# Kernel tuning notes

Measured on AMD Instinct MI355X. Metric: run time of the kernel, lower is better.

## Reference

```python
import jax, jax.numpy as jnp
import numpy as np

N = 8192      # tokens
DIM = 1024    # model dim
E = 8         # num_experts
TOPK = 2      # min(2, num_experts)


def setup_inputs() -> dict:
    key = jax.random.key(0)
    ks = jax.random.split(key, 6)
    def w(k, shape, fan_in):
        return jax.random.normal(k, shape, jnp.float32) / np.float32(np.sqrt(fan_in))
    return {
        "x":   jax.random.normal(ks[0], (N, DIM), jnp.float32),
        # gate MLP: Linear(dim, 2*dim) -> SiLU -> Linear(2*dim, E)
        "Wg1": w(ks[1], (DIM, 2 * DIM), DIM),
        "bg1": jnp.zeros((2 * DIM,), jnp.float32),
        "Wg2": w(ks[2], (2 * DIM, E), 2 * DIM),
        "bg2": jnp.zeros((E,), jnp.float32),
        # experts: SHARED ff1 Linear(dim, 4*dim), per-expert ff2 Linear(4*dim, dim)
        "W1":  w(ks[3], (DIM, 4 * DIM), DIM),
        "b1":  jnp.zeros((4 * DIM,), jnp.float32),
        "W2":  w(ks[4], (E, 4 * DIM, DIM), 4 * DIM),
        "b2":  jnp.zeros((E, DIM), jnp.float32),
    }


def reference(x, Wg1, bg1, Wg2, bg2, W1, b1, W2, b2):
    # gate runs on detached input (x.detach())
    xg = jax.lax.stop_gradient(x)
    gates = jax.nn.silu(xg @ Wg1 + bg1) @ Wg2 + bg2          # [N, E]
    w, idx = jax.lax.top_k(gates, TOPK)                       # [N, K]
    w = jax.nn.softmax(w, axis=-1)                            # softmax over top-k weights
    # shared ff1 hidden, computed once for all experts
    h = jax.nn.silu(x @ W1 + b1)                              # [N, 4*DIM]
    # dense per-expert ff2 over the whole batch (matches original's full-batch expert compute)
    eo = jnp.einsum('nh,ehd->ned', h, W2) + b2                # [N, E, DIM]
    # dispatch/combine: gather selected experts per token, weight and sum
    sel = jnp.take_along_axis(eo, idx[:, :, None], axis=1)    # [N, K, DIM]
    return jnp.sum(w[:, :, None] * sel, axis=1)               # [N, DIM]
```

## Files before the change

### kernel.cpp

```cpp
#include <hip/hip_runtime.h>
#include <hip/hip_bf16.h>
#include <cstddef>

#define N_TOK 8192
#define DIM   1024
#define HG    2048
#define NE    8
#define HEXP  4096

#define BM 128
#define BN 128
#define BK 16
#define THETA 0.05f

typedef __attribute__((ext_vector_type(8))) short bf16x8;
typedef __attribute__((ext_vector_type(4))) float f32x4;

__device__ __forceinline__ float silu_f(float z) {
    return z / (1.0f + expf(-z));
}

__device__ __forceinline__ unsigned short f2bf(float v) {
    unsigned u = __float_as_uint(v);
    unsigned r = (u + 0x7FFFu + ((u >> 16) & 1u)) >> 16;
    return (unsigned short)r;
}

__device__ __forceinline__ float bf2f(unsigned short v) {
    return __uint_as_float((unsigned)v << 16);
}

__device__ __forceinline__ void gl16(const unsigned short* g, unsigned short* l) {
    __builtin_amdgcn_global_load_lds(
        (const __attribute__((address_space(1))) unsigned int*)(const void*)g,
        (__attribute__((address_space(3))) unsigned int*)(void*)l, 16, 0, 0);
}


__global__ __launch_bounds__(256) void conv_x(const float* __restrict__ src,
                                              unsigned short* __restrict__ dst)
{
    const size_t total = (size_t)N_TOK * DIM;
    size_t i = ((size_t)blockIdx.x * 256 + threadIdx.x) * 4;
    const size_t step = (size_t)gridDim.x * 256 * 4;
    for (; i + 3 < total; i += step) {
        float4 v = *(const float4*)(src + i);
        ushort4 o;
        o.x = f2bf(v.x); o.y = f2bf(v.y); o.z = f2bf(v.z); o.w = f2bf(v.w);
        *(ushort4*)(dst + i) = o;
    }
}

__global__ __launch_bounds__(256) void transpose_conv(const float* __restrict__ src,
                                                      unsigned short* __restrict__ dst,
                                                      int R, int C)
{
    __shared__ float tile[64][65];
    const size_t bofs = (size_t)blockIdx.z * R * C;
    const float* s = src + bofs;
    unsigned short* d = dst + bofs;
    const int r0 = blockIdx.y * 64, c0 = blockIdx.x * 64;
    const int t = threadIdx.x;
    #pragma unroll
    for (int i = 0; i < 16; i++) {
        int id = t + i * 256;
        int r = id >> 6, c = id & 63;
        tile[r][c] = s[(size_t)(r0 + r) * C + c0 + c];
    }
    __syncthreads();
    #pragma unroll
    for (int i = 0; i < 16; i++) {
        int id = t + i * 256;
        int c = id >> 6, r = id & 63;
        d[(size_t)(c0 + c) * R + r0 + r] = f2bf(tile[r][c]);
    }
}


#define TBK 64

__global__ __launch_bounds__(256) void gemm_bf16_silu(
    const unsigned short* __restrict__ A,
    const unsigned short* __restrict__ Bt,
    const float* __restrict__ bias,
    unsigned short* __restrict__ C,
    int Nc)
{
    __shared__ __align__(16) unsigned short As[128][TBK];
    __shared__ __align__(16) unsigned short Bs[128][TBK];

    const int tid  = threadIdx.x;
    const int wave = tid >> 6;
    const int lane = tid & 63;
    const int wm = wave >> 1, wn = wave & 1;
    const int l15 = lane & 15;
    const int lk  = lane >> 4;
    const int row0 = blockIdx.y * 128;
    const int col0 = blockIdx.x * 128;

    const int l8  = lane >> 3;
    const int cbs = (lane & 7) ^ l8;
    const unsigned short* pA[4];
    const unsigned short* pB[4];
    #pragma unroll
    for (int i = 0; i < 4; i++) {
        const int r = wave * 32 + i * 8 + l8;
        pA[i] = A  + (size_t)(row0 + r) * DIM + cbs * 8;
        pB[i] = Bt + (size_t)(col0 + r) * DIM + cbs * 8;
    }

    f32x4 acc[4][4] = {};

    for (int k0 = 0; k0 < DIM; k0 += TBK) {
        __syncthreads();
        #pragma unroll
        for (int i = 0; i < 4; i++) {
            gl16(pA[i] + k0, &As[wave * 32 + i * 8][0]);
            gl16(pB[i] + k0, &Bs[wave * 32 + i * 8][0]);
        }
        __syncthreads();

        #pragma unroll
        for (int ks = 0; ks < 2; ks++) {
            bf16x8 af[4], bfr[4];
            const int kb = (ks * 32 + lk * 8) * 2;
            #pragma unroll
            for (int mi = 0; mi < 4; mi++) {
                const int r = wm * 64 + mi * 16 + l15;
                af[mi] = *(const bf16x8*)((const char*)&As[r][0] + (kb ^ ((r & 7) << 4)));
            }
            #pragma unroll
            for (int ni = 0; ni < 4; ni++) {
                const int r = wn * 64 + ni * 16 + l15;
                bfr[ni] = *(const bf16x8*)((const char*)&Bs[r][0] + (kb ^ ((r & 7) << 4)));
            }
            #pragma unroll
            for (int mi = 0; mi < 4; mi++)
                #pragma unroll
                for (int ni = 0; ni < 4; ni++)
                    acc[mi][ni] = __builtin_amdgcn_mfma_f32_16x16x32_bf16(
                        af[mi], bfr[ni], acc[mi][ni], 0, 0, 0);
        }
    }

    #pragma unroll
    for (int ni = 0; ni < 4; ni++) {
        const int gc = col0 + wn * 64 + ni * 16 + l15;
        const float bv = bias[gc];
        #pragma unroll
        for (int mi = 0; mi < 4; mi++) {
            #pragma unroll
            for (int r = 0; r < 4; r++) {
                const int gr = row0 + wm * 64 + mi * 16 + lk * 4 + r;
                C[(size_t)gr * Nc + gc] = f2bf(silu_f(acc[mi][ni][r] + bv));
            }
        }
    }
}


__global__ __launch_bounds__(256) void gate2_topk_flag(
    const unsigned short* __restrict__ g1b, const float* __restrict__ Wg2,
    const float* __restrict__ bg2,
    unsigned* __restrict__ tok_list, float* __restrict__ w_list,
    unsigned* __restrict__ meta, unsigned* __restrict__ flaglist)
{
    const int wid  = threadIdx.x >> 6;
    const int lane = threadIdx.x & 63;
    const int t = blockIdx.x * 4 + wid;
    if (t >= N_TOK) return;

    float acc[NE];
    #pragma unroll
    for (int e = 0; e < NE; e++) acc[e] = 0.0f;

    const unsigned short* g = g1b + (size_t)t * HG;
    for (int kb = lane * 8; kb < HG; kb += 512) {
        ushort4 ga = *(const ushort4*)(g + kb);
        ushort4 gb = *(const ushort4*)(g + kb + 4);
        float gv[8];
        gv[0] = bf2f(ga.x); gv[1] = bf2f(ga.y); gv[2] = bf2f(ga.z); gv[3] = bf2f(ga.w);
        gv[4] = bf2f(gb.x); gv[5] = bf2f(gb.y); gv[6] = bf2f(gb.z); gv[7] = bf2f(gb.w);
        #pragma unroll
        for (int j = 0; j < 8; j++) {
            const float4 wa = *(const float4*)(Wg2 + (size_t)(kb + j) * NE);
            const float4 wb = *(const float4*)(Wg2 + (size_t)(kb + j) * NE + 4);
            acc[0] = fmaf(gv[j], wa.x, acc[0]);
            acc[1] = fmaf(gv[j], wa.y, acc[1]);
            acc[2] = fmaf(gv[j], wa.z, acc[2]);
            acc[3] = fmaf(gv[j], wa.w, acc[3]);
            acc[4] = fmaf(gv[j], wb.x, acc[4]);
            acc[5] = fmaf(gv[j], wb.y, acc[5]);
            acc[6] = fmaf(gv[j], wb.z, acc[6]);
            acc[7] = fmaf(gv[j], wb.w, acc[7]);
        }
    }
    #pragma unroll
    for (int off = 32; off > 0; off >>= 1) {
        #pragma unroll
        for (int e = 0; e < NE; e++)
            acc[e] += __shfl_down(acc[e], off);
    }
    if (lane == 0) {
        float v0 = -3.4e38f, v1 = -3.4e38f, v2 = -3.4e38f;
        int i0 = 0, i1 = 0;
        #pragma unroll
        for (int e = 0; e < NE; e++) {
            const float v = acc[e] + bg2[e];
            if (v > v0)      { v2 = v1; v1 = v0; i1 = i0; v0 = v; i0 = e; }
            else if (v > v1) { v2 = v1; v1 = v; i1 = e; }
            else if (v > v2) { v2 = v; }
        }
        if (v1 - v2 < THETA) {
            const unsigned p = atomicAdd(&meta[17], 1u);
            flaglist[p] = (unsigned)t;
        } else {
            const float e1 = expf(v1 - v0);
            const float inv = 1.0f / (1.0f + e1);
            const unsigned p0 = atomicAdd(&meta[i0], 1u);
            tok_list[i0 * N_TOK + p0] = (unsigned)t;
            w_list [i0 * N_TOK + p0] = inv;
            const unsigned p1 = atomicAdd(&meta[i1], 1u);
            tok_list[i1 * N_TOK + p1] = (unsigned)t;
            w_list [i1 * N_TOK + p1] = e1 * inv;
        }
    }
}

__global__ __launch_bounds__(256) void regate_gemm(
    const float* __restrict__ x, const float* __restrict__ Wg1,
    const float* __restrict__ bg1,
    const unsigned* __restrict__ flaglist, const unsigned* __restrict__ meta,
    float* __restrict__ g1f)
{
    const int nflag = (int)meta[17];
    const int rs = blockIdx.y * BM;
    if (rs >= nflag) return;
    const int re = (rs + BM < nflag) ? rs + BM : nflag;
    const int col0 = blockIdx.x * BN;

    __shared__ float As[BK][BM];
    __shared__ float Bs[BK][BN];

    const int tid = threadIdx.x;
    const int tx = tid & 15;
    const int ty = tid >> 4;
    const int ar = tid >> 2;
    const int ac = (tid & 3) << 2;
    const int br = tid >> 5;
    const int bc = (tid & 31) << 2;

    const int r0 = rs + ar;
    const int r1 = rs + ar + 64;
    const unsigned t0 = flaglist[(r0 < re) ? r0 : rs];
    const unsigned t1 = flaglist[(r1 < re) ? r1 : rs];
    const float* A0 = x + (size_t)t0 * DIM + ac;
    const float* A1 = x + (size_t)t1 * DIM + ac;
    const float* Bp = Wg1 + (size_t)br * HG + col0 + bc;

    float acc[8][8];
    #pragma unroll
    for (int i = 0; i < 8; i++)
        #pragma unroll
        for (int j = 0; j < 8; j++) acc[i][j] = 0.0f;

    for (int k0 = 0; k0 < DIM; k0 += BK) {
        const float4 a0 = *(const float4*)(A0 + k0);
        const float4 a1 = *(const float4*)(A1 + k0);
        const float4 b0 = *(const float4*)(Bp + (size_t)k0 * HG);
        const float4 b1 = *(const float4*)(Bp + (size_t)(k0 + 8) * HG);

        __syncthreads();
        As[ac + 0][ar] = a0.x; As[ac + 1][ar] = a0.y;
        As[ac + 2][ar] = a0.z; As[ac + 3][ar] = a0.w;
        As[ac + 0][ar + 64] = a1.x; As[ac + 1][ar + 64] = a1.y;
        As[ac + 2][ar + 64] = a1.z; As[ac + 3][ar + 64] = a1.w;
        *(float4*)&Bs[br][bc]     = b0;
        *(float4*)&Bs[br + 8][bc] = b1;
        __syncthreads();

        #pragma unroll
        for (int k = 0; k < BK; k++) {
            float a[8], b[8];
            *(float4*)&a[0] = *(const float4*)&As[k][ty * 8];
            *(float4*)&a[4] = *(const float4*)&As[k][ty * 8 + 4];
            *(float4*)&b[0] = *(const float4*)&Bs[k][tx * 8];
            *(float4*)&b[4] = *(const float4*)&Bs[k][tx * 8 + 4];
            #pragma unroll
            for (int i = 0; i < 8; i++)
                #pragma unroll
                for (int j = 0; j < 8; j++)
                    acc[i][j] = fmaf(a[i], b[j], acc[i][j]);
        }
    }

    #pragma unroll
    for (int i = 0; i < 8; i++) {
        const int row = rs + ty * 8 + i;
        if (row < re) {
            const int col = col0 + tx * 8;
            #pragma unroll
            for (int j = 0; j < 8; j++)
                g1f[(size_t)row * HG + col + j] = silu_f(acc[i][j] + bg1[col + j]);
        }
    }
}

__global__ __launch_bounds__(256) void regate_top2(
    const float* __restrict__ g1f, const float* __restrict__ Wg2,
    const float* __restrict__ bg2,
    const unsigned* __restrict__ flaglist,
    unsigned* __restrict__ tok_list, float* __restrict__ w_list,
    unsigned* __restrict__ meta)
{
    const int wid  = threadIdx.x >> 6;
    const int lane = threadIdx.x & 63;
    const int f = blockIdx.x * 4 + wid;
    const int nflag = (int)meta[17];
    if (f >= nflag) return;
    const unsigned t = flaglist[f];

    float acc[NE];
    #pragma unroll
    for (int e = 0; e < NE; e++) acc[e] = 0.0f;

    const float* g = g1f + (size_t)f * HG;
    for (int k = lane; k < HG; k += 64) {
        const float gv = g[k];
        const float4 wa = *(const float4*)(Wg2 + (size_t)k * NE);
        const float4 wb = *(const float4*)(Wg2 + (size_t)k * NE + 4);
        acc[0] = fmaf(gv, wa.x, acc[0]);
        acc[1] = fmaf(gv, wa.y, acc[1]);
        acc[2] = fmaf(gv, wa.z, acc[2]);
        acc[3] = fmaf(gv, wa.w, acc[3]);
        acc[4] = fmaf(gv, wb.x, acc[4]);
        acc[5] = fmaf(gv, wb.y, acc[5]);
        acc[6] = fmaf(gv, wb.z, acc[6]);
        acc[7] = fmaf(gv, wb.w, acc[7]);
    }
    #pragma unroll
    for (int off = 32; off > 0; off >>= 1) {
        #pragma unroll
        for (int e = 0; e < NE; e++)
            acc[e] += __shfl_down(acc[e], off);
    }
    if (lane == 0) {
        float v0 = -3.4e38f, v1 = -3.4e38f;
        int i0 = 0, i1 = 0;
        #pragma unroll
        for (int e = 0; e < NE; e++) {
            const float v = acc[e] + bg2[e];
            if (v > v0) { v1 = v0; i1 = i0; v0 = v; i0 = e; }
            else if (v > v1) { v1 = v; i1 = e; }
        }
        const float e1 = expf(v1 - v0);
        const float inv = 1.0f / (1.0f + e1);
        const unsigned p0 = atomicAdd(&meta[i0], 1u);
        tok_list[i0 * N_TOK + p0] = (unsigned)t;
        w_list [i0 * N_TOK + p0] = inv;
        const unsigned p1 = atomicAdd(&meta[i1], 1u);
        tok_list[i1 * N_TOK + p1] = (unsigned)t;
        w_list [i1 * N_TOK + p1] = e1 * inv;
    }
}

__global__ void build_tiles(unsigned* __restrict__ meta,
                            unsigned* __restrict__ tile_e,
                            unsigned* __restrict__ tile_rs,
                            unsigned* __restrict__ tile_re)
{
    if (threadIdx.x == 0 && blockIdx.x == 0) {
        int nt = 0;
        for (int e = 0; e < NE; e++) {
            const unsigned c = meta[e];
            for (unsigned s = 0; s < c; s += 128) {
                tile_e[nt]  = (unsigned)e;
                tile_rs[nt] = (unsigned)(e * N_TOK) + s;
                unsigned re = s + 128; if (re > c) re = c;
                tile_re[nt] = (unsigned)(e * N_TOK) + re;
                nt++;
            }
        }
        meta[16] = (unsigned)nt;
    }
}

__global__ __launch_bounds__(256) void ff2_mfma(
    const unsigned short* __restrict__ Hb,
    const unsigned short* __restrict__ W2t,
    const float* __restrict__ b2,
    const unsigned* __restrict__ tok_list, const float* __restrict__ w_list,
    const unsigned* __restrict__ meta,
    const unsigned* __restrict__ tile_e, const unsigned* __restrict__ tile_rs,
    const unsigned* __restrict__ tile_re,
    float* __restrict__ out)
{
    const unsigned nt = meta[16];
    if (blockIdx.x >= nt) return;

    const int e  = (int)tile_e[blockIdx.x];
    const int rs = (int)tile_rs[blockIdx.x];
    const int re = (int)tile_re[blockIdx.x];
    const int col0 = blockIdx.y * 128;

    __shared__ __align__(16) unsigned short As[128][TBK];
    __shared__ __align__(16) unsigned short Bs[128][TBK];
    __shared__ unsigned tokr[128];

    const int tid  = threadIdx.x;
    const int wave = tid >> 6;
    const int lane = tid & 63;
    const int wm = wave >> 1, wn = wave & 1;
    const int l15 = lane & 15;
    const int lk  = lane >> 4;

    if (tid < 128)
        tokr[tid] = (rs + tid < re) ? tok_list[rs + tid] : tok_list[rs];
    __syncthreads();

    const unsigned short* Bsrc = W2t + (size_t)e * DIM * HEXP;

    const int l8  = lane >> 3;
    const int cbs = (lane & 7) ^ l8;
    const unsigned short* pA[4];
    const unsigned short* pB[4];
    #pragma unroll
    for (int i = 0; i < 4; i++) {
        const int r = wave * 32 + i * 8 + l8;
        pA[i] = Hb + (size_t)tokr[r] * HEXP + cbs * 8;
        pB[i] = Bsrc + (size_t)(col0 + r) * HEXP + cbs * 8;
    }

    f32x4 acc[4][4] = {};

    for (int k0 = 0; k0 < HEXP; k0 += TBK) {
        __syncthreads();
        #pragma unroll
        for (int i = 0; i < 4; i++) {
            gl16(pA[i] + k0, &As[wave * 32 + i * 8][0]);
            gl16(pB[i] + k0, &Bs[wave * 32 + i * 8][0]);
        }
        __syncthreads();

        #pragma unroll
        for (int ks = 0; ks < 2; ks++) {
            bf16x8 af[4], bfr[4];
            const int kb = (ks * 32 + lk * 8) * 2;
            #pragma unroll
            for (int mi = 0; mi < 4; mi++) {
                const int r = wm * 64 + mi * 16 + l15;
                af[mi] = *(const bf16x8*)((const char*)&As[r][0] + (kb ^ ((r & 7) << 4)));
            }
            #pragma unroll
            for (int ni = 0; ni < 4; ni++) {
                const int r = wn * 64 + ni * 16 + l15;
                bfr[ni] = *(const bf16x8*)((const char*)&Bs[r][0] + (kb ^ ((r & 7) << 4)));
            }
            #pragma unroll
            for (int mi = 0; mi < 4; mi++)
                #pragma unroll
                for (int ni = 0; ni < 4; ni++)
                    acc[mi][ni] = __builtin_amdgcn_mfma_f32_16x16x32_bf16(
                        af[mi], bfr[ni], acc[mi][ni], 0, 0, 0);
        }
    }

    #pragma unroll
    for (int ni = 0; ni < 4; ni++) {
        const int gc = col0 + wn * 64 + ni * 16 + l15;
        const float bv = b2[(size_t)e * DIM + gc];
        #pragma unroll
        for (int mi = 0; mi < 4; mi++) {
            #pragma unroll
            for (int r = 0; r < 4; r++) {
                const int lr = wm * 64 + mi * 16 + lk * 4 + r;
                if (rs + lr < re) {
                    const unsigned tok = tokr[lr];
                    const float w = w_list[rs + lr];
                    atomicAdd(out + (size_t)tok * DIM + gc, w * (acc[mi][ni][r] + bv));
                }
            }
        }
    }
}

extern "C" void kernel_launch(void* const* d_in, const int* in_sizes, int n_in,
                              void* d_out, int out_size, void* d_ws, size_t ws_size,
                              hipStream_t stream)
{
    const float* x   = (const float*)d_in[0];
    const float* Wg1 = (const float*)d_in[1];
    const float* bg1 = (const float*)d_in[2];
    const float* Wg2 = (const float*)d_in[3];
    const float* bg2 = (const float*)d_in[4];
    const float* W1  = (const float*)d_in[5];
    const float* b1  = (const float*)d_in[6];
    const float* W2  = (const float*)d_in[7];
    const float* b2  = (const float*)d_in[8];
    float* out = (float*)d_out;

    char* ws = (char*)d_ws;
    const size_t MB = 1024 * 1024;
    unsigned short* xb   = (unsigned short*)(ws);
    unsigned short* W1t  = (unsigned short*)(ws + 16 * MB);
    unsigned short* Wg1t = (unsigned short*)(ws + 24 * MB);
    unsigned short* g1b  = (unsigned short*)(ws + 28 * MB);
    float*          g1f  = (float*)        (ws + 28 * MB);
    unsigned short* hbuf = (unsigned short*)(ws + 28 * MB);
    unsigned short* W2t  = (unsigned short*)(ws + 92 * MB);
    unsigned* tok_list = (unsigned*)(ws + 156 * MB);
    float*    w_list   = (float*)   (ws + 156 * MB + 65536 * 4);
    unsigned* meta     = (unsigned*)(ws + 156 * MB + 65536 * 8);
    unsigned* tile_e   = meta + 1024;
    unsigned* tile_rs  = meta + 1280;
    unsigned* tile_re  = meta + 1536;
    unsigned* flaglist = meta + 2048;

    (void)hipMemsetAsync(d_out, 0, (size_t)out_size * sizeof(float), stream);
    (void)hipMemsetAsync(meta, 0, 128, stream);

    const dim3 blk(256);
    conv_x<<<dim3(2048), blk, 0, stream>>>(x, xb);
    transpose_conv<<<dim3(HG / 64, DIM / 64, 1), blk, 0, stream>>>(Wg1, Wg1t, DIM, HG);
    gemm_bf16_silu<<<dim3(HG / 128, N_TOK / 128), blk, 0, stream>>>(xb, Wg1t, bg1, g1b, HG);
    gate2_topk_flag<<<dim3(N_TOK / 4), blk, 0, stream>>>(
        g1b, Wg2, bg2, tok_list, w_list, meta, flaglist);
    regate_gemm<<<dim3(HG / BN, N_TOK / BM), blk, 0, stream>>>(
        x, Wg1, bg1, flaglist, meta, g1f);
    regate_top2<<<dim3(N_TOK / 4), blk, 0, stream>>>(
        g1f, Wg2, bg2, flaglist, tok_list, w_list, meta);
    build_tiles<<<dim3(1), dim3(64), 0, stream>>>(meta, tile_e, tile_rs, tile_re);
    transpose_conv<<<dim3(HEXP / 64, DIM / 64, 1), blk, 0, stream>>>(W1, W1t, DIM, HEXP);
    gemm_bf16_silu<<<dim3(HEXP / 128, N_TOK / 128), blk, 0, stream>>>(xb, W1t, b1, hbuf, HEXP);
    transpose_conv<<<dim3(DIM / 64, HEXP / 64, NE), blk, 0, stream>>>(W2, W2t, HEXP, DIM);
    ff2_mfma<<<dim3(N_TOK * 2 / 128 + NE, DIM / 128), blk, 0, stream>>>(
        hbuf, W2t, b2, tok_list, w_list, meta, tile_e, tile_rs, tile_re, out);
}
```

Before: 1.091 ms.

## Double-buffer LDS tiles in bf16 GEMMs and swap ff2 grid axes

Both bf16 GEMM kernels now double-buffer their LDS tiles with a K-step of 32. The next tile's global-to-LDS load is issued before the MFMA work on the current one, so each iteration needs only one barrier instead of two. The LDS swizzle is changed to fit the narrower rows. The ff2 launch swaps grid axes so the blocks sharing one expert tile run next to each other, which should improve L2 reuse of the gathered H rows. The risks are more loop iterations with less MFMA work per barrier, and depending on the async-load ordering and the barrier placement being correct.

After: 1.072 ms. About the same (-1.8%).

```diff
diff --git a/kernel.cpp b/kernel.cpp
--- a/kernel.cpp
+++ b/kernel.cpp
@@ -77,7 +77,7 @@
 }
 
 
-#define TBK 64
+#define TBK 32
 
 __global__ __launch_bounds__(256) void gemm_bf16_silu(
     const unsigned short* __restrict__ A,
@@ -86,8 +86,8 @@
     unsigned short* __restrict__ C,
     int Nc)
 {
-    __shared__ __align__(16) unsigned short As[128][TBK];
-    __shared__ __align__(16) unsigned short Bs[128][TBK];
+    __shared__ __align__(16) unsigned short As[2][128][TBK];
+    __shared__ __align__(16) unsigned short Bs[2][128][TBK];
 
     const int tid  = threadIdx.x;
     const int wave = tid >> 6;
@@ -98,49 +98,58 @@
     const int row0 = blockIdx.y * 128;
     const int col0 = blockIdx.x * 128;
 
-    const int l8  = lane >> 3;
-    const int cbs = (lane & 7) ^ l8;
-    const unsigned short* pA[4];
-    const unsigned short* pB[4];
-    #pragma unroll
-    for (int i = 0; i < 4; i++) {
-        const int r = wave * 32 + i * 8 + l8;
+    const int srow = lane >> 2;
+    const int cbs  = (lane & 3) ^ ((lane >> 3) & 3);
+    const unsigned short* pA[2];
+    const unsigned short* pB[2];
+    #pragma unroll
+    for (int i = 0; i < 2; i++) {
+        const int r = wave * 32 + i * 16 + srow;
         pA[i] = A  + (size_t)(row0 + r) * DIM + cbs * 8;
         pB[i] = Bt + (size_t)(col0 + r) * DIM + cbs * 8;
     }
 
     f32x4 acc[4][4] = {};
 
+    #pragma unroll
+    for (int i = 0; i < 2; i++) {
+        gl16(pA[i], &As[0][wave * 32 + i * 16][0]);
+        gl16(pB[i], &Bs[0][wave * 32 + i * 16][0]);
+    }
+    __syncthreads();
+
+    int db = 0;
     for (int k0 = 0; k0 < DIM; k0 += TBK) {
+        if (k0 + TBK < DIM) {
+            #pragma unroll
+            for (int i = 0; i < 2; i++) {
+                gl16(pA[i] + k0 + TBK, &As[db ^ 1][wave * 32 + i * 16][0]);
+                gl16(pB[i] + k0 + TBK, &Bs[db ^ 1][wave * 32 + i * 16][0]);
+            }
+        }
+        __builtin_amdgcn_sched_barrier(0);
+
+        bf16x8 af[4], bfr[4];
+        const int kb = lk * 16;
+        #pragma unroll
+        for (int mi = 0; mi < 4; mi++) {
+            const int r = wm * 64 + mi * 16 + l15;
+            af[mi] = *(const bf16x8*)((const char*)&As[db][r][0] + (kb ^ (((r >> 1) & 3) << 4)));
+        }
+        #pragma unroll
+        for (int ni = 0; ni < 4; ni++) {
+            const int r = wn * 64 + ni * 16 + l15;
+            bfr[ni] = *(const bf16x8*)((const char*)&Bs[db][r][0] + (kb ^ (((r >> 1) & 3) << 4)));
+        }
+        #pragma unroll
+        for (int mi = 0; mi < 4; mi++)
+            #pragma unroll
+            for (int ni = 0; ni < 4; ni++)
+                acc[mi][ni] = __builtin_amdgcn_mfma_f32_16x16x32_bf16(
+                    af[mi], bfr[ni], acc[mi][ni], 0, 0, 0);
+
         __syncthreads();
-        #pragma unroll
-        for (int i = 0; i < 4; i++) {
-            gl16(pA[i] + k0, &As[wave * 32 + i * 8][0]);
-            gl16(pB[i] + k0, &Bs[wave * 32 + i * 8][0]);
-        }
-        __syncthreads();
-
-        #pragma unroll
-        for (int ks = 0; ks < 2; ks++) {
-            bf16x8 af[4], bfr[4];
-            const int kb = (ks * 32 + lk * 8) * 2;
-            #pragma unroll
-            for (int mi = 0; mi < 4; mi++) {
-                const int r = wm * 64 + mi * 16 + l15;
-                af[mi] = *(const bf16x8*)((const char*)&As[r][0] + (kb ^ ((r & 7) << 4)));
-            }
-            #pragma unroll
-            for (int ni = 0; ni < 4; ni++) {
-                const int r = wn * 64 + ni * 16 + l15;
-                bfr[ni] = *(const bf16x8*)((const char*)&Bs[r][0] + (kb ^ ((r & 7) << 4)));
-            }
-            #pragma unroll
-            for (int mi = 0; mi < 4; mi++)
-                #pragma unroll
-                for (int ni = 0; ni < 4; ni++)
-                    acc[mi][ni] = __builtin_amdgcn_mfma_f32_16x16x32_bf16(
-                        af[mi], bfr[ni], acc[mi][ni], 0, 0, 0);
-        }
+        db ^= 1;
     }
 
     #pragma unroll
@@ -396,15 +405,15 @@
     float* __restrict__ out)
 {
     const unsigned nt = meta[16];
-    if (blockIdx.x >= nt) return;
-
-    const int e  = (int)tile_e[blockIdx.x];
-    const int rs = (int)tile_rs[blockIdx.x];
-    const int re = (int)tile_re[blockIdx.x];
-    const int col0 = blockIdx.y * 128;
-
-    __shared__ __align__(16) unsigned short As[128][TBK];
-    __shared__ __align__(16) unsigned short Bs[128][TBK];
+    if (blockIdx.y >= nt) return;
+
+    const int e  = (int)tile_e[blockIdx.y];
+    const int rs = (int)tile_rs[blockIdx.y];
+    const int re = (int)tile_re[blockIdx.y];
+    const int col0 = blockIdx.x * 128;
+
+    __shared__ __align__(16) unsigned short As[2][128][TBK];
+    __shared__ __align__(16) unsigned short Bs[2][128][TBK];
     __shared__ unsigned tokr[128];
 
     const int tid  = threadIdx.x;
@@ -420,49 +429,58 @@
 
     const unsigned short* Bsrc = W2t + (size_t)e * DIM * HEXP;
 
-    const int l8  = lane >> 3;
-    const int cbs = (lane & 7) ^ l8;
-    const unsigned short* pA[4];
-    const unsigned short* pB[4];
-    #pragma unroll
-    for (int i = 0; i < 4; i++) {
-        const int r = wave * 32 + i * 8 + l8;
+    const int srow = lane >> 2;
+    const int cbs  = (lane & 3) ^ ((lane >> 3) & 3);
+    const unsigned short* pA[2];
+    const unsigned short* pB[2];
+    #pragma unroll
+    for (int i = 0; i < 2; i++) {
+        const int r = wave * 32 + i * 16 + srow;
         pA[i] = Hb + (size_t)tokr[r] * HEXP + cbs * 8;
         pB[i] = Bsrc + (size_t)(col0 + r) * HEXP + cbs * 8;
     }
 
     f32x4 acc[4][4] = {};
 
+    #pragma unroll
+    for (int i = 0; i < 2; i++) {
+        gl16(pA[i], &As[0][wave * 32 + i * 16][0]);
+        gl16(pB[i], &Bs[0][wave * 32 + i * 16][0]);
+    }
+    __syncthreads();
+
+    int db = 0;
     for (int k0 = 0; k0 < HEXP; k0 += TBK) {
+        if (k0 + TBK < HEXP) {
+            #pragma unroll
+            for (int i = 0; i < 2; i++) {
+                gl16(pA[i] + k0 + TBK, &As[db ^ 1][wave * 32 + i * 16][0]);
+                gl16(pB[i] + k0 + TBK, &Bs[db ^ 1][wave * 32 + i * 16][0]);
+            }
+        }
+        __builtin_amdgcn_sched_barrier(0);
+
+        bf16x8 af[4], bfr[4];
+        const int kb = lk * 16;
+        #pragma unroll
+        for (int mi = 0; mi < 4; mi++) {
+            const int r = wm * 64 + mi * 16 + l15;
+            af[mi] = *(const bf16x8*)((const char*)&As[db][r][0] + (kb ^ (((r >> 1) & 3) << 4)));
+        }
+        #pragma unroll
+        for (int ni = 0; ni < 4; ni++) {
+            const int r = wn * 64 + ni * 16 + l15;
+            bfr[ni] = *(const bf16x8*)((const char*)&Bs[db][r][0] + (kb ^ (((r >> 1) & 3) << 4)));
+        }
+        #pragma unroll
+        for (int mi = 0; mi < 4; mi++)
+            #pragma unroll
+            for (int ni = 0; ni < 4; ni++)
+                acc[mi][ni] = __builtin_amdgcn_mfma_f32_16x16x32_bf16(
+                    af[mi], bfr[ni], acc[mi][ni], 0, 0, 0);
+
         __syncthreads();
-        #pragma unroll
-        for (int i = 0; i < 4; i++) {
-            gl16(pA[i] + k0, &As[wave * 32 + i * 8][0]);
-            gl16(pB[i] + k0, &Bs[wave * 32 + i * 8][0]);
-        }
-        __syncthreads();
-
-        #pragma unroll
-        for (int ks = 0; ks < 2; ks++) {
-            bf16x8 af[4], bfr[4];
-            const int kb = (ks * 32 + lk * 8) * 2;
-            #pragma unroll
-            for (int mi = 0; mi < 4; mi++) {
-                const int r = wm * 64 + mi * 16 + l15;
-                af[mi] = *(const bf16x8*)((const char*)&As[r][0] + (kb ^ ((r & 7) << 4)));
-            }
-            #pragma unroll
-            for (int ni = 0; ni < 4; ni++) {
-                const int r = wn * 64 + ni * 16 + l15;
-                bfr[ni] = *(const bf16x8*)((const char*)&Bs[r][0] + (kb ^ ((r & 7) << 4)));
-            }
-            #pragma unroll
-            for (int mi = 0; mi < 4; mi++)
-                #pragma unroll
-                for (int ni = 0; ni < 4; ni++)
-                    acc[mi][ni] = __builtin_amdgcn_mfma_f32_16x16x32_bf16(
-                        af[mi], bfr[ni], acc[mi][ni], 0, 0, 0);
-        }
+        db ^= 1;
     }
 
     #pragma unroll
@@ -533,6 +551,6 @@
     transpose_conv<<<dim3(HEXP / 64, DIM / 64, 1), blk, 0, stream>>>(W1, W1t, DIM, HEXP);
     gemm_bf16_silu<<<dim3(HEXP / 128, N_TOK / 128), blk, 0, stream>>>(xb, W1t, b1, hbuf, HEXP);
     transpose_conv<<<dim3(DIM / 64, HEXP / 64, NE), blk, 0, stream>>>(W2, W2t, HEXP, DIM);
-    ff2_mfma<<<dim3(N_TOK * 2 / 128 + NE, DIM / 128), blk, 0, stream>>>(
+    ff2_mfma<<<dim3(DIM / 128, N_TOK * 2 / 128 + NE), blk, 0, stream>>>(
         hbuf, W2t, b2, tok_list, w_list, meta, tile_e, tile_rs, tile_re, out);
 }
```
